# Performance work log

Hardware: AMD Instinct MI355X
Metric: run time of the kernel (lower is better)

Reference implementation:

```python
import jax, jax.numpy as jnp
import numpy as np

H, HD, C = 16, 64, 64            # num_heads, head_dim, mini_batch_size
BASE_LR = 1.0
EPS = 1e-6                        # ttt LN eps (ln_fwd / ln_fused_l2_bwd)


def _l2norm(x):
    return x / jnp.maximum(jnp.linalg.norm(x, axis=-1, keepdims=True), 1e-12)


def _ln_fwd(x, g, b):
    mu = x.mean(-1, keepdims=True)
    var = x.var(-1, keepdims=True)
    return g * ((x - mu) * jax.lax.rsqrt(var + EPS)) + b


def _ln_l2_bwd(x, tgt, g, b):
    # gradient of ||LN(x)*g+b - tgt||^2 / 2 wrt x
    D = x.shape[-1]
    mu = x.mean(-1, keepdims=True)
    var = x.var(-1, keepdims=True)
    std = jnp.sqrt(var + EPS)
    xh = (x - mu) / std
    gout = (g * xh + b) - tgt
    gxh = gout * g
    return (D * gxh - gxh.sum(-1, keepdims=True) - xh * (gxh * xh).sum(-1, keepdims=True)) / (D * std)


def setup_inputs() -> dict:
    key = jax.random.key(0)
    ks = jax.random.split(key, 12)
    B, L, D = 4, 8192, 1024
    std = 0.02
    return {
        'hidden_states': jax.random.normal(ks[0], (B, L, D), jnp.float32),
        'wq_w': jax.random.normal(ks[1], (D, D), jnp.float32) * std,
        'wq_b': jnp.zeros((D,), jnp.float32),
        'wk_w': jax.random.normal(ks[2], (D, D), jnp.float32) * std,
        'wk_b': jnp.zeros((D,), jnp.float32),
        'wv_w': jax.random.normal(ks[3], (D, D), jnp.float32) * std,
        'wv_b': jnp.zeros((D,), jnp.float32),
        'wo_w': jax.random.normal(ks[4], (D, D), jnp.float32) * std,
        'wo_b': jnp.zeros((D,), jnp.float32),
        'ttt_norm_weight': jnp.ones((H, HD), jnp.float32),
        'ttt_norm_bias': jnp.zeros((H, HD), jnp.float32),
        'ttt_lr_weight': jax.random.normal(ks[5], (H, 1, D), jnp.float32) * std,
        'ttt_lr_bias': jnp.zeros((H, 1), jnp.float32),
        'W1': jax.random.normal(ks[6], (H, HD, HD), jnp.float32) * std,
        'b1': jnp.zeros((H, 1, HD), jnp.float32),
        'post_norm_w': jnp.ones((D,), jnp.float32),
        'post_norm_b': jnp.zeros((D,), jnp.float32),
    }


def _forward(hidden_states, wq_w, wq_b, wk_w, wk_b, wv_w, wv_b, wo_w, wo_b,
             ttt_norm_weight, ttt_norm_bias, ttt_lr_weight, ttt_lr_bias,
             W1, b1, post_norm_w, post_norm_b):
    B, L, D = hidden_states.shape
    NC = L // C
    XQ = (hidden_states @ wq_w.T + wq_b).reshape(B, L, H, HD)
    XK = (hidden_states @ wk_w.T + wk_b).reshape(B, L, H, HD)
    XV = (hidden_states @ wv_w.T + wv_b).reshape(B, L, H, HD)
    XQ = _l2norm(XQ)
    XK = _l2norm(XK)
    # ln_reconstruction_target (uses sample std, ddof=1, eps=1e-5 on std)
    d = XV - XK
    mu = d.mean(-1, keepdims=True)
    sd = d.std(-1, keepdims=True, ddof=1)
    XV = ttt_norm_weight[None, None] * ((d - mu) / (sd + 1e-5)) + ttt_norm_bias[None, None] + XK
    # reshape to mini-batches: [B,H,NC,C,HD]
    Xmb = hidden_states.reshape(B, NC, C, D)
    to_mb = lambda t: t.transpose(0, 2, 1, 3).reshape(B, H, NC, C, HD)
    XQ, XK, XV = to_mb(XQ), to_mb(XK), to_mb(XV)
    # eta: sigmoid lr gate per token, row-broadcast over mini-batch
    ttt_lr = jax.nn.sigmoid(jnp.einsum('bnkc,hdc->bhnkd', Xmb, ttt_lr_weight)
                            + ttt_lr_bias.reshape(1, H, 1, 1, 1))     # [B,H,NC,C,1]
    eta = jnp.swapaxes(ttt_lr, -1, -2) * (BASE_LR / HD / C)           # [B,H,NC,1,C]
    mask = jnp.tril(jnp.ones((C, C), hidden_states.dtype))
    g = ttt_norm_weight[None, :, None, :]
    bta = ttt_norm_bias[None, :, None, :]
    W0 = jnp.broadcast_to(W1[None], (B, H, HD, HD))
    b0 = jnp.broadcast_to(b1[None], (B, H, 1, HD))

    def step(carry, xs):
        W, bvec = carry
        xq, xk, xv, eta_row = xs                      # eta_row: [B,H,1,C]
        Z1 = xk @ W + bvec                            # [B,H,C,HD]
        grad = _ln_l2_bwd(Z1, xv - xk, g, bta)        # [B,H,C,HD]
        Attn = mask * jnp.einsum('bhid,bhjd->bhij', xq, xk)   # [B,H,C,C]
        eta_full = jnp.broadcast_to(eta_row, Attn.shape)      # [B,H,C,C]
        b1_bar = bvec - (mask * eta_full) @ grad              # [B,H,C,HD]
        Z1_bar = xq @ W - (eta_full * Attn) @ grad + b1_bar
        last_eta = eta_full[..., -1, :, None]                 # [B,H,C,1]
        W_new = W - jnp.einsum('bhcd,bhce->bhde', last_eta * xk, grad)
        b_new = bvec - (last_eta * grad).sum(-2, keepdims=True)
        out = xq + _ln_fwd(Z1_bar, g, bta)
        return (W_new, b_new), out

    xs = (jnp.moveaxis(XQ, 2, 0), jnp.moveaxis(XK, 2, 0),
          jnp.moveaxis(XV, 2, 0), jnp.moveaxis(eta, 2, 0))
    _, outs = jax.lax.scan(step, (W0, b0), xs)        # outs: [NC,B,H,C,HD]
    y = jnp.moveaxis(outs, 0, 2).reshape(B, H, L, HD).transpose(0, 2, 1, 3).reshape(B, L, D)
    # post LayerNorm (eps=1e-6) + output projection
    mu2 = y.mean(-1, keepdims=True)
    var2 = y.var(-1, keepdims=True)
    y = post_norm_w * ((y - mu2) * jax.lax.rsqrt(var2 + 1e-6)) + post_norm_b
    return y @ wo_w.T + wo_b


def reference(hidden_states, wq_w, wq_b, wk_w, wk_b, wv_w, wv_b, wo_w, wo_b,
              ttt_norm_weight, ttt_norm_bias, ttt_lr_weight, ttt_lr_bias,
              W1, b1, post_norm_w, post_norm_b):
    return _forward(hidden_states, wq_w, wq_b, wk_w, wk_b, wv_w, wv_b, wo_w, wo_b,
                    ttt_norm_weight, ttt_norm_bias, ttt_lr_weight, ttt_lr_bias,
                    W1, b1, post_norm_w, post_norm_b)
```

## Files before the change

kernel.cpp:

```cpp
#include <hip/hip_runtime.h>


typedef __attribute__((ext_vector_type(8))) short short8;
typedef __attribute__((ext_vector_type(4))) float f32x4;
typedef __attribute__((ext_vector_type(4))) unsigned short us4;

__device__ __forceinline__ float bf2f(unsigned short s) {
  union { unsigned int u; float f; } c;
  c.u = ((unsigned int)s) << 16;
  return c.f;
}
__device__ __forceinline__ unsigned short f2bf(float f) {
  union { float f; unsigned int u; } c;
  c.f = f;
  unsigned int u = c.u;
  return (unsigned short)((u + 0x7FFFu + ((u >> 16) & 1u)) >> 16);
}

__device__ __forceinline__ void gload_lds16(const void* g, void* l) {
  __builtin_amdgcn_global_load_lds(
      (const __attribute__((address_space(1))) unsigned int*)g,
      (__attribute__((address_space(3))) unsigned int*)l, 16, 0, 0);
}

__device__ __forceinline__ float dpp16_sum(float x) {
  int v = __float_as_int(x);
  x += __int_as_float(__builtin_amdgcn_update_dpp(v, v, 0xB1, 0xF, 0xF, true));
  v = __float_as_int(x);
  x += __int_as_float(__builtin_amdgcn_update_dpp(v, v, 0x4E, 0xF, 0xF, true));
  v = __float_as_int(x);
  x += __int_as_float(__builtin_amdgcn_update_dpp(v, v, 0x141, 0xF, 0xF, true));
  v = __float_as_int(x);
  x += __int_as_float(__builtin_amdgcn_update_dpp(v, v, 0x140, 0xF, 0xF, true));
  return x;
}

__device__ __forceinline__ void barrier_fast() {
  __builtin_amdgcn_sched_barrier(0);
  asm volatile("s_waitcnt lgkmcnt(0)" ::: "memory");
  __builtin_amdgcn_s_barrier();
  asm volatile("" ::: "memory");
  __builtin_amdgcn_sched_barrier(0);
}
__device__ __forceinline__ void bar_nowait() {
  __builtin_amdgcn_sched_barrier(0);
  asm volatile("" ::: "memory");
  __builtin_amdgcn_s_barrier();
  asm volatile("" ::: "memory");
  __builtin_amdgcn_sched_barrier(0);
}

__global__ __launch_bounds__(256) void cvt_f32_bf16(
    const float* __restrict__ in, unsigned short* __restrict__ out, long n) {
  long i = ((long)blockIdx.x * 256 + threadIdx.x) * 4;
  if (i + 3 < n) {
    float4 v = *(const float4*)&in[i];
    us4 o = { f2bf(v.x), f2bf(v.y), f2bf(v.z), f2bf(v.w) };
    *(us4*)&out[i] = o;
  }
}

__global__ __launch_bounds__(256) void build_wcat(
    const float* __restrict__ wq, const float* __restrict__ wk,
    const float* __restrict__ wv, const float* __restrict__ lrw,
    const float* __restrict__ wqb, const float* __restrict__ wkb,
    const float* __restrict__ wvb, const float* __restrict__ lrb,
    unsigned short* __restrict__ Wcat, float* __restrict__ biasc) {
  int i = blockIdx.x * 256 + threadIdx.x;
  int row = i >> 10, col = i & 1023;
  int h = row >> 8, o = row & 255;
  float v;
  if (o < 64)        v = wq[(h * 64 + o) * 1024 + col];
  else if (o < 128)  v = wk[(h * 64 + o - 64) * 1024 + col];
  else if (o < 192)  v = wv[(h * 64 + o - 128) * 1024 + col];
  else if (o == 192) v = lrw[h * 1024 + col];
  else               v = 0.f;
  Wcat[i] = f2bf(v);
  if (i < 4096) {
    int hh = i >> 8, oo = i & 255;
    float bv;
    if (oo < 64)        bv = wqb[hh * 64 + oo];
    else if (oo < 128)  bv = wkb[hh * 64 + oo - 64];
    else if (oo < 192)  bv = wvb[hh * 64 + oo - 128];
    else if (oo == 192) bv = lrb[hh];
    else                bv = 0.f;
    biasc[i] = bv;
  }
}


__global__ __launch_bounds__(512, 1) void gemm256_qkv(
    const unsigned short* __restrict__ A, const unsigned short* __restrict__ B,
    const float* __restrict__ bias, const float* __restrict__ tnw,
    const float* __restrict__ tnb, unsigned short* __restrict__ XQn,
    unsigned short* __restrict__ XKn, unsigned short* __restrict__ TGT,
    float* __restrict__ eta, long M, long K) {
  __shared__ __align__(16) unsigned short g_lds[49152];
  char* ldsc = (char*)g_lds;
  const int tid = threadIdx.x, lane = tid & 63, wid = tid >> 6;
  const int wm = wid >> 2, wn = wid & 3;
  const int l15 = lane & 15, lg = lane >> 4;
  const int NTILN = 16;

  unsigned nwg = gridDim.x, bid = blockIdx.x;
  unsigned cpx = nwg >> 3;
  unsigned swz = (bid & 7) * cpx + (bid >> 3);
  unsigned nidx = swz % (unsigned)NTILN, midx = swz / (unsigned)NTILN;
  const long m0 = (long)midx * 256, n0 = (long)nidx * 256;
  const long ldab = K * 2;

  const int srow = wid * 16 + (lane >> 2);
  const int scol = ((lane & 3) * 16) ^ (((lane >> 3) & 3) << 4);
  const int sdst = wid * 1024;
  const char* Ab = (const char*)A;
  const char* Bb = (const char*)B;

  const int acol = (lg * 16) ^ (((l15 >> 1) & 3) << 4);
  const int aro = (wm * 128 + l15) * 64 + acol;
  const int bro = 16384 + (wn * 64 + l15) * 64 + acol;

#define STG_A(tt, h, bb)                                                      \
  gload_lds16(Ab + (size_t)(m0 + (h) * 128 + srow) * ldab + (size_t)(tt) * 64 \
                  + scol,                                                     \
              ldsc + (bb) * 32768 + (h) * 8192 + sdst)
#define STG_B(tt, h, bb)                                                      \
  gload_lds16(Bb + (size_t)(n0 + (h) * 128 + srow) * ldab + (size_t)(tt) * 64 \
                  + scol,                                                     \
              ldsc + (bb) * 32768 + 16384 + (h) * 8192 + sdst)

  f32x4 acc[8][4];
#pragma unroll
  for (int m = 0; m < 8; ++m)
#pragma unroll
    for (int n = 0; n < 4; ++n) acc[m][n] = (f32x4){0.f, 0.f, 0.f, 0.f};

  const int NT = (int)(K >> 5);

  STG_A(0, 0, 0); STG_A(0, 1, 0); STG_B(0, 0, 0); STG_B(0, 1, 0);
  STG_A(1, 0, 1); STG_A(1, 1, 1); STG_B(1, 0, 1); STG_B(1, 1, 1);
  asm volatile("s_waitcnt vmcnt(4)" ::: "memory");
  bar_nowait();

  int buf = 0, sb = 2;
#pragma unroll 1
  for (int t = 0; t < NT; ++t) {
    if (t + 2 < NT) {
      STG_A(t + 2, 0, sb); STG_A(t + 2, 1, sb);
      STG_B(t + 2, 0, sb); STG_B(t + 2, 1, sb);
    }
    const char* ab = ldsc + buf * 32768 + aro;
    const char* bb2 = ldsc + buf * 32768 + bro;
    short8 av[8], bv[4];
#pragma unroll
    for (int i = 0; i < 8; ++i) av[i] = *(const short8*)(ab + i * 1024);
#pragma unroll
    for (int nf = 0; nf < 4; ++nf) bv[nf] = *(const short8*)(bb2 + nf * 1024);
    __builtin_amdgcn_s_setprio(1);
#pragma unroll
    for (int i = 0; i < 8; ++i)
#pragma unroll
      for (int nf = 0; nf < 4; ++nf)
        acc[i][nf] = __builtin_amdgcn_mfma_f32_16x16x32_bf16(av[i], bv[nf],
                                                             acc[i][nf], 0, 0, 0);
    __builtin_amdgcn_s_setprio(0);
    asm volatile("s_waitcnt vmcnt(4)" ::: "memory");
    bar_nowait();
    buf = (buf == 2) ? 0 : buf + 1;
    sb = (sb == 2) ? 0 : sb + 1;
  }
#undef STG_A
#undef STG_B

  const int h = (int)nidx;
  float bcol[4], twv[4], tbv[4];
#pragma unroll
  for (int nf = 0; nf < 4; ++nf) {
    bcol[nf] = bias[n0 + wn * 64 + nf * 16 + l15];
    twv[nf] = tnw[h * 64 + nf * 16 + l15];
    tbv[nf] = tnb[h * 64 + nf * 16 + l15];
  }
  __syncthreads();
  unsigned short* kn_s = g_lds;

  if (wn == 0) {
#pragma unroll
    for (int mf = 0; mf < 8; ++mf)
#pragma unroll
      for (int j = 0; j < 4; ++j) {
        float v[4], s2 = 0.f;
#pragma unroll
        for (int nf = 0; nf < 4; ++nf) {
          v[nf] = acc[mf][nf][j] + bcol[nf];
          s2 += v[nf] * v[nf];
        }
        s2 = dpp16_sum(s2);
        float rn = 1.f / fmaxf(sqrtf(s2), 1e-12f);
        size_t tt = (size_t)(m0 + wm * 128 + mf * 16 + lg * 4 + j);
#pragma unroll
        for (int nf = 0; nf < 4; ++nf)
          XQn[tt * 1024 + h * 64 + nf * 16 + l15] = f2bf(v[nf] * rn);
      }
  } else if (wn == 1) {
#pragma unroll
    for (int mf = 0; mf < 8; ++mf)
#pragma unroll
      for (int j = 0; j < 4; ++j) {
        float v[4], s2 = 0.f;
#pragma unroll
        for (int nf = 0; nf < 4; ++nf) {
          v[nf] = acc[mf][nf][j] + bcol[nf];
          s2 += v[nf] * v[nf];
        }
        s2 = dpp16_sum(s2);
        float rn = 1.f / fmaxf(sqrtf(s2), 1e-12f);
        size_t tt = (size_t)(m0 + wm * 128 + mf * 16 + lg * 4 + j);
        int lr_ = wm * 128 + mf * 16 + lg * 4 + j;
#pragma unroll
        for (int nf = 0; nf < 4; ++nf) {
          unsigned short kb = f2bf(v[nf] * rn);
          XKn[tt * 1024 + h * 64 + nf * 16 + l15] = kb;
          kn_s[lr_ * 72 + nf * 16 + l15] = kb;
        }
      }
  }
  __syncthreads();
  if (wn == 2) {
#pragma unroll
    for (int mf = 0; mf < 8; ++mf)
#pragma unroll
      for (int j = 0; j < 4; ++j) {
        int lr_ = wm * 128 + mf * 16 + lg * 4 + j;
        float dv[4], s1 = 0.f, s2 = 0.f;
#pragma unroll
        for (int nf = 0; nf < 4; ++nf) {
          float kn = bf2f(kn_s[lr_ * 72 + nf * 16 + l15]);
          dv[nf] = acc[mf][nf][j] + bcol[nf] - kn;
          s1 += dv[nf];
          s2 += dv[nf] * dv[nf];
        }
        s1 = dpp16_sum(s1);
        s2 = dpp16_sum(s2);
        float mu = s1 * 0.015625f;
        float var1 = fmaxf(s2 - 64.f * mu * mu, 0.f) * (1.f / 63.f);
        float rs = 1.f / (sqrtf(var1) + 1e-5f);
        size_t tt = (size_t)(m0 + wm * 128 + mf * 16 + lg * 4 + j);
#pragma unroll
        for (int nf = 0; nf < 4; ++nf)
          TGT[tt * 1024 + h * 64 + nf * 16 + l15] =
              f2bf(twv[nf] * ((dv[nf] - mu) * rs) + tbv[nf]);
      }
  } else if (wn == 3 && l15 == 0) {
#pragma unroll
    for (int mf = 0; mf < 8; ++mf)
#pragma unroll
      for (int j = 0; j < 4; ++j) {
        size_t tt = (size_t)(m0 + wm * 128 + mf * 16 + lg * 4 + j);
        float lgt = acc[mf][0][j] + bcol[0];
        float sig = 1.f / (1.f + expf(-lgt));
        eta[((tt >> 13) * 16 + h) * 8192 + (tt & 8191)] = sig * (1.f / 4096.f);
      }
  }
}

template <int WRITE_BF16>
__global__ __launch_bounds__(512, 1) void gemm256(
    const unsigned short* __restrict__ A, const unsigned short* __restrict__ B,
    const float* __restrict__ bias, void* __restrict__ Cout,
    long M, long N, long K, int NTILN, long ldc) {
  __shared__ __align__(16) unsigned short g_lds[49152];
  char* ldsc = (char*)g_lds;
  const int tid = threadIdx.x, lane = tid & 63, wid = tid >> 6;
  const int wm = wid >> 2, wn = wid & 3;
  const int l15 = lane & 15, lg = lane >> 4;

  unsigned nwg = gridDim.x, bid = blockIdx.x;
  unsigned cpx = nwg >> 3;
  unsigned swz = (bid & 7) * cpx + (bid >> 3);
  unsigned nidx = swz % (unsigned)NTILN, midx = swz / (unsigned)NTILN;
  const long m0 = (long)midx * 256, n0 = (long)nidx * 256;
  const long ldab = K * 2;

  const int srow = wid * 16 + (lane >> 2);
  const int scol = ((lane & 3) * 16) ^ (((lane >> 3) & 3) << 4);
  const int sdst = wid * 1024;
  const char* Ab = (const char*)A;
  const char* Bb = (const char*)B;

  const int acol = (lg * 16) ^ (((l15 >> 1) & 3) << 4);
  const int aro = (wm * 128 + l15) * 64 + acol;
  const int bro = 16384 + (wn * 64 + l15) * 64 + acol;

#define STG_A(tt, h, bb)                                                      \
  gload_lds16(Ab + (size_t)(m0 + (h) * 128 + srow) * ldab + (size_t)(tt) * 64 \
                  + scol,                                                     \
              ldsc + (bb) * 32768 + (h) * 8192 + sdst)
#define STG_B(tt, h, bb)                                                      \
  gload_lds16(Bb + (size_t)(n0 + (h) * 128 + srow) * ldab + (size_t)(tt) * 64 \
                  + scol,                                                     \
              ldsc + (bb) * 32768 + 16384 + (h) * 8192 + sdst)

  f32x4 acc[8][4];
#pragma unroll
  for (int m = 0; m < 8; ++m)
#pragma unroll
    for (int n = 0; n < 4; ++n) acc[m][n] = (f32x4){0.f, 0.f, 0.f, 0.f};

  const int NT = (int)(K >> 5);

  STG_A(0, 0, 0); STG_A(0, 1, 0); STG_B(0, 0, 0); STG_B(0, 1, 0);
  STG_A(1, 0, 1); STG_A(1, 1, 1); STG_B(1, 0, 1); STG_B(1, 1, 1);
  asm volatile("s_waitcnt vmcnt(4)" ::: "memory");
  bar_nowait();

  int buf = 0, sb = 2;
#pragma unroll 1
  for (int t = 0; t < NT; ++t) {
    if (t + 2 < NT) {
      STG_A(t + 2, 0, sb); STG_A(t + 2, 1, sb);
      STG_B(t + 2, 0, sb); STG_B(t + 2, 1, sb);
    }
    const char* ab = ldsc + buf * 32768 + aro;
    const char* bb2 = ldsc + buf * 32768 + bro;
    short8 av[8], bv[4];
#pragma unroll
    for (int i = 0; i < 8; ++i) av[i] = *(const short8*)(ab + i * 1024);
#pragma unroll
    for (int nf = 0; nf < 4; ++nf) bv[nf] = *(const short8*)(bb2 + nf * 1024);
    __builtin_amdgcn_s_setprio(1);
#pragma unroll
    for (int i = 0; i < 8; ++i)
#pragma unroll
      for (int nf = 0; nf < 4; ++nf)
        acc[i][nf] = __builtin_amdgcn_mfma_f32_16x16x32_bf16(av[i], bv[nf],
                                                             acc[i][nf], 0, 0, 0);
    __builtin_amdgcn_s_setprio(0);
    asm volatile("s_waitcnt vmcnt(4)" ::: "memory");
    bar_nowait();
    buf = (buf == 2) ? 0 : buf + 1;
    sb = (sb == 2) ? 0 : sb + 1;
  }
#undef STG_A
#undef STG_B

#pragma unroll
  for (int mf = 0; mf < 8; ++mf) {
    long r0 = m0 + wm * 128 + mf * 16 + lg * 4;
#pragma unroll
    for (int nf = 0; nf < 4; ++nf) {
      long c = n0 + wn * 64 + nf * 16 + l15;
      float bvv = bias ? bias[c] : 0.f;
#pragma unroll
      for (int j = 0; j < 4; ++j) {
        float v = acc[mf][nf][j] + bvv;
        if (WRITE_BF16)
          ((unsigned short*)Cout)[(r0 + j) * ldc + c] = f2bf(v);
        else
          ((float*)Cout)[(r0 + j) * ldc + c] = v;
      }
    }
  }
}

__global__ __launch_bounds__(512, 1) void ttt_scan(
    const unsigned short* __restrict__ XQ, const unsigned short* __restrict__ XK,
    const unsigned short* __restrict__ TG, const float* __restrict__ eta_buf,
    const float* __restrict__ W1, const float* __restrict__ b1,
    const float* __restrict__ tnw, const float* __restrict__ tnb,
    float* __restrict__ y) {
  const int bh = blockIdx.x;
  const int b = bh >> 4, h = bh & 15;
  const int tid = threadIdx.x;
  const int lane = tid & 63, wid = tid >> 6;
  const bool isA = wid < 4;
  const int q = wid & 3;
  const int l15 = lane & 15, lg = lane >> 4;

  __shared__ __align__(16) unsigned short xq_s[2][64 * 72];
  __shared__ __align__(16) unsigned short tg_s[2][64 * 72];
  __shared__ __align__(16) unsigned short xk_s[2][64 * 72];
  __shared__ __align__(16) unsigned short gc_s[64 * 72];
  __shared__ __align__(16) unsigned short gradT[64 * 72];
  __shared__ __align__(16) unsigned short xkTe[64 * 72];
  __shared__ __align__(16) unsigned short WT_b[2][64 * 72];
  __shared__ float eta_s[2][64];
  __shared__ float bpart[4][64];

  const size_t tokb = (size_t)b * 8192;
  const int col0 = h * 64;
  const int rr_ = q * 16 + (lane >> 3);
  const int c8_ = (lane & 7) * 8;

  short8 pA0[2], pA1[2], pB0[2];
  float peta = 0.f;
  float bstv[4], gwv[4], gbv[4];
  f32x4 Wreg[4];

  if (isA) {
#pragma unroll
    for (int n = 0; n < 4; ++n) {
      int e = n * 16 + l15;
      bstv[n] = b1[h * 64 + e];
      gwv[n] = tnw[h * 64 + e];
      gbv[n] = tnb[h * 64 + e];
    }
#pragma unroll
    for (int j = 0; j < 2; ++j) {
      size_t g = (tokb + rr_ + j * 8) * 1024 + col0 + c8_;
      pA0[j] = *(const short8*)&XQ[g];
      pA1[j] = *(const short8*)&TG[g];
    }
#pragma unroll
    for (int j = 0; j < 2; ++j) {
      int rr = rr_ + j * 8;
      *(short8*)&xq_s[0][rr * 72 + c8_] = pA0[j];
      *(short8*)&tg_s[0][rr * 72 + c8_] = pA1[j];
    }
#pragma unroll
    for (int j = 0; j < 2; ++j) {
      size_t g = (tokb + 64 + rr_ + j * 8) * 1024 + col0 + c8_;
      pA0[j] = *(const short8*)&XQ[g];
      pA1[j] = *(const short8*)&TG[g];
    }
  } else {
#pragma unroll
    for (int j = 0; j < 2; ++j)
      pB0[j] = *(const short8*)&XK[(tokb + rr_ + j * 8) * 1024 + col0 + c8_];
#pragma unroll
    for (int j = 0; j < 2; ++j)
      *(short8*)&xk_s[0][(rr_ + j * 8) * 72 + c8_] = pB0[j];
#pragma unroll
    for (int j = 0; j < 2; ++j)
      pB0[j] = *(const short8*)&XK[(tokb + 64 + rr_ + j * 8) * 1024 + col0 + c8_];
#pragma unroll
    for (int n = 0; n < 4; ++n)
#pragma unroll
      for (int jj = 0; jj < 4; ++jj) {
        int d = q * 16 + lg * 4 + jj, e = n * 16 + l15;
        float w = W1[h * 4096 + d * 64 + e];
        Wreg[n][jj] = w;
        WT_b[0][e * 72 + d] = f2bf(w);
      }
    if (wid == 4) {
      eta_s[0][lane] = eta_buf[(size_t)bh * 8192 + lane];
      peta = eta_buf[(size_t)bh * 8192 + 64 + lane];
    }
  }
  __syncthreads();

  for (int nc = 0; nc < 128; ++nc) {
    const int p = nc & 1;
    const unsigned short* WTc = WT_b[p];
    unsigned short* WTn = WT_b[p ^ 1];

    if (isA) {
      if (nc) {
#pragma unroll
        for (int n = 0; n < 4; ++n) {
          int e = n * 16 + l15;
          bstv[n] -= bpart[0][e] + bpart[1][e] + bpart[2][e] + bpart[3][e];
        }
      }
      if (nc + 1 < 128) {
#pragma unroll
        for (int j = 0; j < 2; ++j) {
          int rr = rr_ + j * 8;
          *(short8*)&xq_s[p ^ 1][rr * 72 + c8_] = pA0[j];
          *(short8*)&tg_s[p ^ 1][rr * 72 + c8_] = pA1[j];
        }
      }
      if (nc + 2 < 128) {
#pragma unroll
        for (int j = 0; j < 2; ++j) {
          size_t g = (tokb + (nc + 2) * 64 + rr_ + j * 8) * 1024 + col0 + c8_;
          pA0[j] = *(const short8*)&XQ[g];
          pA1[j] = *(const short8*)&TG[g];
        }
      }
      f32x4 accZ[4];
#pragma unroll
      for (int n = 0; n < 4; ++n)
        accZ[n] = (f32x4){bstv[n], bstv[n], bstv[n], bstv[n]};
      __builtin_amdgcn_s_setprio(1);
#pragma unroll
      for (int kk = 0; kk < 2; ++kk) {
        const int ko = kk * 32 + lg * 8;
        short8 a_xk = *(const short8*)&xk_s[p][(q * 16 + l15) * 72 + ko];
#pragma unroll
        for (int n = 0; n < 4; ++n) {
          short8 b_w = *(const short8*)&WTc[(n * 16 + l15) * 72 + ko];
          accZ[n] = __builtin_amdgcn_mfma_f32_16x16x32_bf16(a_xk, b_w, accZ[n], 0, 0, 0);
        }
      }
      __builtin_amdgcn_s_setprio(0);
      float grv[4][4];
#pragma unroll
      for (int j = 0; j < 4; ++j) {
        const int r = q * 16 + lg * 4 + j;
        float z[4], s1 = 0.f, s2 = 0.f;
#pragma unroll
        for (int n = 0; n < 4; ++n) {
          z[n] = accZ[n][j];
          s1 += z[n];
          s2 += z[n] * z[n];
        }
        s1 = dpp16_sum(s1);
        s2 = dpp16_sum(s2);
        float mu = s1 * 0.015625f;
        float var = s2 * 0.015625f - mu * mu;
        float rstd = rsqrtf(var + 1e-6f);
        float xh[4], gx[4], s3 = 0.f, s4 = 0.f;
#pragma unroll
        for (int n = 0; n < 4; ++n) {
          xh[n] = (z[n] - mu) * rstd;
          float tg = bf2f(tg_s[p][r * 72 + n * 16 + l15]);
          float go = gwv[n] * xh[n] + gbv[n] - tg;
          gx[n] = go * gwv[n];
          s3 += gx[n];
          s4 += gx[n] * xh[n];
        }
        s3 = dpp16_sum(s3);
        s4 = dpp16_sum(s4);
#pragma unroll
        for (int n = 0; n < 4; ++n)
          grv[n][j] = (64.f * gx[n] - s3 - xh[n] * s4) * rstd * 0.015625f;
      }
#pragma unroll
      for (int n = 0; n < 4; ++n) {
        us4 pk = {f2bf(grv[n][0]), f2bf(grv[n][1]), f2bf(grv[n][2]),
                  f2bf(grv[n][3])};
        *(us4*)&gradT[(n * 16 + l15) * 72 + q * 16 + lg * 4] = pk;
      }
    } else {
      if (nc + 1 < 128) {
#pragma unroll
        for (int j = 0; j < 2; ++j)
          *(short8*)&xk_s[p ^ 1][(rr_ + j * 8) * 72 + c8_] = pB0[j];
        if (wid == 4) eta_s[p ^ 1][lane] = peta;
      }
      if (nc + 2 < 128) {
#pragma unroll
        for (int j = 0; j < 2; ++j)
          pB0[j] = *(const short8*)
              &XK[(tokb + (nc + 2) * 64 + rr_ + j * 8) * 1024 + col0 + c8_];
        if (wid == 4) peta = eta_buf[(size_t)bh * 8192 + (nc + 2) * 64 + lane];
      }
#pragma unroll
      for (int it = 0; it < 4; ++it) {
        int c0 = q * 16 + it * 4;
        us4 pk;
#pragma unroll
        for (int u = 0; u < 4; ++u)
          pk[u] = f2bf(-eta_s[p][c0 + u] * bf2f(xk_s[p][(c0 + u) * 72 + lane]));
        *(us4*)&xkTe[lane * 72 + c0] = pk;
      }
      f32x4 accA[4];
#pragma unroll
      for (int n = 0; n < 4; ++n) accA[n] = (f32x4){0.f, 0.f, 0.f, 0.f};
      __builtin_amdgcn_s_setprio(1);
#pragma unroll
      for (int kk = 0; kk < 2; ++kk) {
        const int ko = kk * 32 + lg * 8;
        short8 a_xq = *(const short8*)&xq_s[p][(q * 16 + l15) * 72 + ko];
#pragma unroll
        for (int n = 0; n < 4; ++n) {
          short8 b_k = *(const short8*)&xk_s[p][(n * 16 + l15) * 72 + ko];
          accA[n] = __builtin_amdgcn_mfma_f32_16x16x32_bf16(a_xq, b_k, accA[n], 0, 0, 0);
        }
      }
      __builtin_amdgcn_s_setprio(0);
#pragma unroll
      for (int j = 0; j < 4; ++j) {
        const int r = q * 16 + lg * 4 + j;
#pragma unroll
        for (int n = 0; n < 4; ++n) {
          int cj = n * 16 + l15;
          float v = (cj <= r) ? (-eta_s[p][cj] * (1.f + accA[n][j])) : 0.f;
          gc_s[r * 72 + cj] = f2bf(v);
        }
      }
    }
    barrier_fast();

    if (isA) {
      f32x4 accZb[4];
#pragma unroll
      for (int n = 0; n < 4; ++n)
        accZb[n] = (f32x4){bstv[n], bstv[n], bstv[n], bstv[n]};
      __builtin_amdgcn_s_setprio(1);
#pragma unroll
      for (int kk = 0; kk < 2; ++kk) {
        const int ko = kk * 32 + lg * 8;
        short8 a_xq = *(const short8*)&xq_s[p][(q * 16 + l15) * 72 + ko];
        short8 a_gc = *(const short8*)&gc_s[(q * 16 + l15) * 72 + ko];
#pragma unroll
        for (int n = 0; n < 4; ++n) {
          short8 b_w = *(const short8*)&WTc[(n * 16 + l15) * 72 + ko];
          short8 b_g = *(const short8*)&gradT[(n * 16 + l15) * 72 + ko];
          accZb[n] = __builtin_amdgcn_mfma_f32_16x16x32_bf16(a_xq, b_w, accZb[n], 0, 0, 0);
          accZb[n] = __builtin_amdgcn_mfma_f32_16x16x32_bf16(a_gc, b_g, accZb[n], 0, 0, 0);
        }
      }
      __builtin_amdgcn_s_setprio(0);
#pragma unroll
      for (int j = 0; j < 4; ++j) {
        const int r = q * 16 + lg * 4 + j;
        float z[4], s1 = 0.f, s2 = 0.f;
#pragma unroll
        for (int n = 0; n < 4; ++n) {
          z[n] = accZb[n][j];
          s1 += z[n];
          s2 += z[n] * z[n];
        }
        s1 = dpp16_sum(s1);
        s2 = dpp16_sum(s2);
        float mu = s1 * 0.015625f;
        float var = s2 * 0.015625f - mu * mu;
        float rstd = rsqrtf(var + 1e-6f);
        size_t gbase = (tokb + nc * 64 + r) * 1024 + col0;
#pragma unroll
        for (int n = 0; n < 4; ++n) {
          int e = n * 16 + l15;
          float ov = bf2f(xq_s[p][r * 72 + e]) + gwv[n] * ((z[n] - mu) * rstd) + gbv[n];
          y[gbase + e] = ov;
        }
      }
    } else {
      short8 a_ke[2], b_g[2][4];
#pragma unroll
      for (int kk = 0; kk < 2; ++kk) {
        const int ko = kk * 32 + lg * 8;
        a_ke[kk] = *(const short8*)&xkTe[(q * 16 + l15) * 72 + ko];
#pragma unroll
        for (int n = 0; n < 4; ++n)
          b_g[kk][n] = *(const short8*)&gradT[(n * 16 + l15) * 72 + ko];
      }
      f32x4 accW[4];
#pragma unroll
      for (int n = 0; n < 4; ++n) accW[n] = Wreg[n];
      __builtin_amdgcn_s_setprio(1);
#pragma unroll
      for (int kk = 0; kk < 2; ++kk)
#pragma unroll
        for (int n = 0; n < 4; ++n)
          accW[n] = __builtin_amdgcn_mfma_f32_16x16x32_bf16(a_ke[kk], b_g[kk][n],
                                                            accW[n], 0, 0, 0);
      __builtin_amdgcn_s_setprio(0);
#pragma unroll
      for (int n = 0; n < 4; ++n) {
        Wreg[n] = accW[n];
        us4 pk = {f2bf(accW[n][0]), f2bf(accW[n][1]), f2bf(accW[n][2]),
                  f2bf(accW[n][3])};
        *(us4*)&WTn[(n * 16 + l15) * 72 + q * 16 + lg * 4] = pk;
      }
      {
        float s = 0.f;
#pragma unroll
        for (int it = 0; it < 4; ++it) {
          us4 gv = *(const us4*)&gradT[lane * 72 + q * 16 + it * 4];
#pragma unroll
          for (int u = 0; u < 4; ++u)
            s += eta_s[p][q * 16 + it * 4 + u] * bf2f(gv[u]);
        }
        bpart[q][lane] = s;
      }
    }
    barrier_fast();
  }
}

__global__ __launch_bounds__(256) void postnorm(
    const float* __restrict__ yv, const float* __restrict__ pw,
    const float* __restrict__ pb, unsigned short* __restrict__ yn) {
  int t = blockIdx.x;
  int tid = threadIdx.x, lane = tid & 63, wid = tid >> 6;
  const float* row = yv + (size_t)t * 1024;
  float4 v = *(const float4*)&row[tid * 4];
  float s1 = v.x + v.y + v.z + v.w;
  float s2 = v.x * v.x + v.y * v.y + v.z * v.z + v.w * v.w;
#pragma unroll
  for (int o = 1; o < 64; o <<= 1) {
    s1 += __shfl_xor(s1, o);
    s2 += __shfl_xor(s2, o);
  }
  __shared__ float r1[4], r2[4];
  if (lane == 0) {
    r1[wid] = s1;
    r2[wid] = s2;
  }
  __syncthreads();
  s1 = r1[0] + r1[1] + r1[2] + r1[3];
  s2 = r2[0] + r2[1] + r2[2] + r2[3];
  float mu = s1 * (1.f / 1024.f);
  float var = s2 * (1.f / 1024.f) - mu * mu;
  float rstd = rsqrtf(var + 1e-6f);
  int c = tid * 4;
  us4 o4 = {f2bf(pw[c] * ((v.x - mu) * rstd) + pb[c]),
            f2bf(pw[c + 1] * ((v.y - mu) * rstd) + pb[c + 1]),
            f2bf(pw[c + 2] * ((v.z - mu) * rstd) + pb[c + 2]),
            f2bf(pw[c + 3] * ((v.w - mu) * rstd) + pb[c + 3])};
  *(us4*)&yn[(size_t)t * 1024 + c] = o4;
}

extern "C" void kernel_launch(void* const* d_in, const int* in_sizes, int n_in,
                              void* d_out, int out_size, void* d_ws,
                              size_t ws_size, hipStream_t stream) {
  const float* hs  = (const float*)d_in[0];
  const float* wqw = (const float*)d_in[1];
  const float* wqb = (const float*)d_in[2];
  const float* wkw = (const float*)d_in[3];
  const float* wkb = (const float*)d_in[4];
  const float* wvw = (const float*)d_in[5];
  const float* wvb = (const float*)d_in[6];
  const float* wow = (const float*)d_in[7];
  const float* wob = (const float*)d_in[8];
  const float* tnw = (const float*)d_in[9];
  const float* tnb = (const float*)d_in[10];
  const float* lrw = (const float*)d_in[11];
  const float* lrb = (const float*)d_in[12];
  const float* W1  = (const float*)d_in[13];
  const float* b1  = (const float*)d_in[14];
  const float* pnw = (const float*)d_in[15];
  const float* pnb = (const float*)d_in[16];

  const size_t OFF_XQ    = 0;
  const size_t OFF_XK    = 67108864;
  const size_t OFF_TGT   = 134217728;
  const size_t OFF_ETA   = 201326592;
  const size_t OFF_WOBF  = OFF_ETA + 2097152;
  const size_t OFF_HSBF  = OFF_WOBF + 2097152;
  const size_t OFF_WCAT  = OFF_HSBF + 67108864;
  const size_t OFF_BIASC = OFF_WCAT + 8388608;
  const size_t OFF_YV    = OFF_HSBF;
  const size_t NEEDED_A  = OFF_BIASC + 16384;
  const size_t NEEDED_B  = OFF_YV + 134217728;
  const size_t NEEDED    = NEEDED_A > NEEDED_B ? NEEDED_A : NEEDED_B;
  if (ws_size < NEEDED) return;

  char* ws = (char*)d_ws;
  unsigned short* XQn   = (unsigned short*)(ws + OFF_XQ);
  unsigned short* ynorm = (unsigned short*)(ws + OFF_XQ);
  unsigned short* XKn   = (unsigned short*)(ws + OFF_XK);
  unsigned short* TGT   = (unsigned short*)(ws + OFF_TGT);
  float* eta_buf        = (float*)(ws + OFF_ETA);
  unsigned short* wo_bf = (unsigned short*)(ws + OFF_WOBF);
  unsigned short* hs_bf = (unsigned short*)(ws + OFF_HSBF);
  unsigned short* Wcat  = (unsigned short*)(ws + OFF_WCAT);
  float* biasc          = (float*)(ws + OFF_BIASC);
  float* yv             = (float*)(ws + OFF_YV);

  cvt_f32_bf16<<<32768, 256, 0, stream>>>(hs, hs_bf, 33554432L);
  build_wcat<<<16384, 256, 0, stream>>>(wqw, wkw, wvw, lrw, wqb, wkb, wvb, lrb,
                                        Wcat, biasc);
  cvt_f32_bf16<<<1024, 256, 0, stream>>>(wow, wo_bf, 1048576L);
  gemm256_qkv<<<2048, 512, 0, stream>>>(hs_bf, Wcat, biasc, tnw, tnb,
                                        XQn, XKn, TGT, eta_buf, 32768L, 1024L);
  ttt_scan<<<64, 512, 0, stream>>>(XQn, XKn, TGT, eta_buf, W1, b1, tnw, tnb, yv);
  postnorm<<<32768, 256, 0, stream>>>(yv, pnw, pnb, ynorm);
  gemm256<0><<<512, 512, 0, stream>>>(ynorm, wo_bf, wob, d_out,
                                      32768L, 1024L, 1024L, 4, 1024L);
}
```

Baseline: 889.1 us.

## Fuse QKV GEMM and TTT scan into one persistent kernel with progress flags

Merges the QKV projection GEMM and the sequential TTT scan into a single launch. The first 64 blocks run the per-(batch, head) scan and spin on per-row-tile atomic progress counters, while the remaining blocks compute GEMM tiles in an order matched to the scan's consumption. This lets the serial scan overlap the GEMM instead of waiting for it to finish. The scan output is also stored as bf16 instead of fp32, halving the traffic into the post-norm. Risks include spin-wait deadlock if scan blocks occupy CUs before producer blocks get scheduled, and a small precision loss on the intermediate y.

```diff
diff --git a/kernel.cpp b/kernel.cpp
--- a/kernel.cpp
+++ b/kernel.cpp
@@ -15,6 +15,11 @@
   c.f = f;
   unsigned int u = c.u;
   return (unsigned short)((u + 0x7FFFu + ((u >> 16) & 1u)) >> 16);
+}
+__device__ __forceinline__ unsigned cvtpk(float lo, float hi) {
+  unsigned r;
+  asm("v_cvt_pk_bf16_f32 %0, %1, %2" : "=v"(r) : "v"(lo), "v"(hi));
+  return r;
 }
 
 __device__ __forceinline__ void gload_lds16(const void* g, void* l) {
@@ -88,177 +93,511 @@
   }
 }
 
-
-__global__ __launch_bounds__(512, 1) void gemm256_qkv(
+__global__ __launch_bounds__(512, 1) void qkv_scan(
     const unsigned short* __restrict__ A, const unsigned short* __restrict__ B,
     const float* __restrict__ bias, const float* __restrict__ tnw,
     const float* __restrict__ tnb, unsigned short* __restrict__ XQn,
     unsigned short* __restrict__ XKn, unsigned short* __restrict__ TGT,
-    float* __restrict__ eta, long M, long K) {
-  __shared__ __align__(16) unsigned short g_lds[49152];
-  char* ldsc = (char*)g_lds;
-  const int tid = threadIdx.x, lane = tid & 63, wid = tid >> 6;
-  const int wm = wid >> 2, wn = wid & 3;
+    float* __restrict__ eta_buf, const float* __restrict__ W1,
+    const float* __restrict__ b1, unsigned short* __restrict__ y,
+    unsigned int* __restrict__ prog) {
+  __shared__ __align__(16) char smem[102912];
+  const int tid = threadIdx.x;
+  const int lane = tid & 63, wid = tid >> 6;
   const int l15 = lane & 15, lg = lane >> 4;
-  const int NTILN = 16;
-
-  unsigned nwg = gridDim.x, bid = blockIdx.x;
-  unsigned cpx = nwg >> 3;
-  unsigned swz = (bid & 7) * cpx + (bid >> 3);
-  unsigned nidx = swz % (unsigned)NTILN, midx = swz / (unsigned)NTILN;
-  const long m0 = (long)midx * 256, n0 = (long)nidx * 256;
-  const long ldab = K * 2;
-
-  const int srow = wid * 16 + (lane >> 2);
-  const int scol = ((lane & 3) * 16) ^ (((lane >> 3) & 3) << 4);
-  const int sdst = wid * 1024;
-  const char* Ab = (const char*)A;
-  const char* Bb = (const char*)B;
-
-  const int acol = (lg * 16) ^ (((l15 >> 1) & 3) << 4);
-  const int aro = (wm * 128 + l15) * 64 + acol;
-  const int bro = 16384 + (wn * 64 + l15) * 64 + acol;
-
-#define STG_A(tt, h, bb)                                                      \
-  gload_lds16(Ab + (size_t)(m0 + (h) * 128 + srow) * ldab + (size_t)(tt) * 64 \
-                  + scol,                                                     \
-              ldsc + (bb) * 32768 + (h) * 8192 + sdst)
-#define STG_B(tt, h, bb)                                                      \
-  gload_lds16(Bb + (size_t)(n0 + (h) * 128 + srow) * ldab + (size_t)(tt) * 64 \
-                  + scol,                                                     \
-              ldsc + (bb) * 32768 + 16384 + (h) * 8192 + sdst)
-
-  f32x4 acc[8][4];
-#pragma unroll
-  for (int m = 0; m < 8; ++m)
-#pragma unroll
-    for (int n = 0; n < 4; ++n) acc[m][n] = (f32x4){0.f, 0.f, 0.f, 0.f};
-
-  const int NT = (int)(K >> 5);
-
-  STG_A(0, 0, 0); STG_A(0, 1, 0); STG_B(0, 0, 0); STG_B(0, 1, 0);
-  STG_A(1, 0, 1); STG_A(1, 1, 1); STG_B(1, 0, 1); STG_B(1, 1, 1);
-  asm volatile("s_waitcnt vmcnt(4)" ::: "memory");
-  bar_nowait();
-
-  int buf = 0, sb = 2;
-#pragma unroll 1
-  for (int t = 0; t < NT; ++t) {
-    if (t + 2 < NT) {
-      STG_A(t + 2, 0, sb); STG_A(t + 2, 1, sb);
-      STG_B(t + 2, 0, sb); STG_B(t + 2, 1, sb);
-    }
-    const char* ab = ldsc + buf * 32768 + aro;
-    const char* bb2 = ldsc + buf * 32768 + bro;
-    short8 av[8], bv[4];
-#pragma unroll
-    for (int i = 0; i < 8; ++i) av[i] = *(const short8*)(ab + i * 1024);
-#pragma unroll
-    for (int nf = 0; nf < 4; ++nf) bv[nf] = *(const short8*)(bb2 + nf * 1024);
-    __builtin_amdgcn_s_setprio(1);
-#pragma unroll
-    for (int i = 0; i < 8; ++i)
-#pragma unroll
-      for (int nf = 0; nf < 4; ++nf)
-        acc[i][nf] = __builtin_amdgcn_mfma_f32_16x16x32_bf16(av[i], bv[nf],
-                                                             acc[i][nf], 0, 0, 0);
-    __builtin_amdgcn_s_setprio(0);
+
+  if (blockIdx.x >= 64) {
+    char* ldsc = smem;
+    const int bid2 = blockIdx.x - 64;
+    const int w = bid2 >> 6, rem = bid2 & 63, bb = rem >> 4, h = rem & 15;
+    const int mprog = bb * 32 + w;
+    const long m0 = (long)mprog * 256;
+    const long n0 = (long)h * 256;
+    const long K = 1024, ldab = 2048;
+
+    const int wm = wid >> 2, wn = wid & 3;
+    const int srow = wid * 16 + (lane >> 2);
+    const int scol = ((lane & 3) * 16) ^ (((lane >> 3) & 3) << 4);
+    const int sdst = wid * 1024;
+    const char* Ab = (const char*)A;
+    const char* Bb = (const char*)B;
+    const int acol = (lg * 16) ^ (((l15 >> 1) & 3) << 4);
+    const int aro = (wm * 128 + l15) * 64 + acol;
+    const int bro = 16384 + (wn * 64 + l15) * 64 + acol;
+
+#define STG_A(tt, hh, bbu)                                                    \
+  gload_lds16(Ab + (size_t)(m0 + (hh) * 128 + srow) * ldab +                  \
+                  (size_t)(tt) * 64 + scol,                                   \
+              ldsc + (bbu) * 32768 + (hh) * 8192 + sdst)
+#define STG_B(tt, hh, bbu)                                                    \
+  gload_lds16(Bb + (size_t)(n0 + (hh) * 128 + srow) * ldab +                  \
+                  (size_t)(tt) * 64 + scol,                                   \
+              ldsc + (bbu) * 32768 + 16384 + (hh) * 8192 + sdst)
+
+    f32x4 acc[8][4];
+#pragma unroll
+    for (int m = 0; m < 8; ++m)
+#pragma unroll
+      for (int n = 0; n < 4; ++n) acc[m][n] = (f32x4){0.f, 0.f, 0.f, 0.f};
+
+    const int NT = (int)(K >> 5);
+    STG_A(0, 0, 0); STG_A(0, 1, 0); STG_B(0, 0, 0); STG_B(0, 1, 0);
+    STG_A(1, 0, 1); STG_A(1, 1, 1); STG_B(1, 0, 1); STG_B(1, 1, 1);
     asm volatile("s_waitcnt vmcnt(4)" ::: "memory");
     bar_nowait();
-    buf = (buf == 2) ? 0 : buf + 1;
-    sb = (sb == 2) ? 0 : sb + 1;
-  }
+
+    int buf = 0, sb = 2;
+#pragma unroll 1
+    for (int t = 0; t < NT; ++t) {
+      if (t + 2 < NT) {
+        STG_A(t + 2, 0, sb); STG_A(t + 2, 1, sb);
+        STG_B(t + 2, 0, sb); STG_B(t + 2, 1, sb);
+      }
+      const char* ab = ldsc + buf * 32768 + aro;
+      const char* bb2 = ldsc + buf * 32768 + bro;
+      short8 av[8], bv[4];
+#pragma unroll
+      for (int i = 0; i < 8; ++i) av[i] = *(const short8*)(ab + i * 1024);
+#pragma unroll
+      for (int nf = 0; nf < 4; ++nf) bv[nf] = *(const short8*)(bb2 + nf * 1024);
+      __builtin_amdgcn_s_setprio(1);
+#pragma unroll
+      for (int i = 0; i < 8; ++i)
+#pragma unroll
+        for (int nf = 0; nf < 4; ++nf)
+          acc[i][nf] = __builtin_amdgcn_mfma_f32_16x16x32_bf16(
+              av[i], bv[nf], acc[i][nf], 0, 0, 0);
+      __builtin_amdgcn_s_setprio(0);
+      if (t < NT - 2)
+        asm volatile("s_waitcnt vmcnt(4)" ::: "memory");
+      else
+        asm volatile("s_waitcnt vmcnt(0)" ::: "memory");
+      bar_nowait();
+      buf = (buf == 2) ? 0 : buf + 1;
+      sb = (sb == 2) ? 0 : sb + 1;
+    }
 #undef STG_A
 #undef STG_B
 
-  const int h = (int)nidx;
-  float bcol[4], twv[4], tbv[4];
-#pragma unroll
-  for (int nf = 0; nf < 4; ++nf) {
-    bcol[nf] = bias[n0 + wn * 64 + nf * 16 + l15];
-    twv[nf] = tnw[h * 64 + nf * 16 + l15];
-    tbv[nf] = tnb[h * 64 + nf * 16 + l15];
+    float bcol[4], twv[4], tbv[4];
+#pragma unroll
+    for (int nf = 0; nf < 4; ++nf) {
+      bcol[nf] = bias[n0 + wn * 64 + nf * 16 + l15];
+      twv[nf] = tnw[h * 64 + nf * 16 + l15];
+      tbv[nf] = tnb[h * 64 + nf * 16 + l15];
+    }
+    __syncthreads();
+    unsigned short* kn_s = (unsigned short*)smem;
+
+    if (wn == 0) {
+#pragma unroll
+      for (int mf = 0; mf < 8; ++mf)
+#pragma unroll
+        for (int j = 0; j < 4; ++j) {
+          float v[4], s2 = 0.f;
+#pragma unroll
+          for (int nf = 0; nf < 4; ++nf) {
+            v[nf] = acc[mf][nf][j] + bcol[nf];
+            s2 += v[nf] * v[nf];
+          }
+          s2 = dpp16_sum(s2);
+          float rn = 1.f / fmaxf(sqrtf(s2), 1e-12f);
+          size_t tt = (size_t)(m0 + wm * 128 + mf * 16 + lg * 4 + j);
+#pragma unroll
+          for (int nf = 0; nf < 4; ++nf)
+            XQn[tt * 1024 + h * 64 + nf * 16 + l15] = f2bf(v[nf] * rn);
+        }
+    } else if (wn == 1) {
+#pragma unroll
+      for (int mf = 0; mf < 8; ++mf)
+#pragma unroll
+        for (int j = 0; j < 4; ++j) {
+          float v[4], s2 = 0.f;
+#pragma unroll
+          for (int nf = 0; nf < 4; ++nf) {
+            v[nf] = acc[mf][nf][j] + bcol[nf];
+            s2 += v[nf] * v[nf];
+          }
+          s2 = dpp16_sum(s2);
+          float rn = 1.f / fmaxf(sqrtf(s2), 1e-12f);
+          size_t tt = (size_t)(m0 + wm * 128 + mf * 16 + lg * 4 + j);
+          int lr_ = wm * 128 + mf * 16 + lg * 4 + j;
+#pragma unroll
+          for (int nf = 0; nf < 4; ++nf) {
+            unsigned short kb = f2bf(v[nf] * rn);
+            XKn[tt * 1024 + h * 64 + nf * 16 + l15] = kb;
+            kn_s[lr_ * 72 + nf * 16 + l15] = kb;
+          }
+        }
+    }
+    __syncthreads();
+    if (wn == 2) {
+#pragma unroll
+      for (int mf = 0; mf < 8; ++mf)
+#pragma unroll
+        for (int j = 0; j < 4; ++j) {
+          int lr_ = wm * 128 + mf * 16 + lg * 4 + j;
+          float dv[4], s1 = 0.f, s2 = 0.f;
+#pragma unroll
+          for (int nf = 0; nf < 4; ++nf) {
+            float kn = bf2f(kn_s[lr_ * 72 + nf * 16 + l15]);
+            dv[nf] = acc[mf][nf][j] + bcol[nf] - kn;
+            s1 += dv[nf];
+            s2 += dv[nf] * dv[nf];
+          }
+          s1 = dpp16_sum(s1);
+          s2 = dpp16_sum(s2);
+          float mu = s1 * 0.015625f;
+          float var1 = fmaxf(s2 - 64.f * mu * mu, 0.f) * (1.f / 63.f);
+          float rs = 1.f / (sqrtf(var1) + 1e-5f);
+          size_t tt = (size_t)(m0 + wm * 128 + mf * 16 + lg * 4 + j);
+#pragma unroll
+          for (int nf = 0; nf < 4; ++nf)
+            TGT[tt * 1024 + h * 64 + nf * 16 + l15] =
+                f2bf(twv[nf] * ((dv[nf] - mu) * rs) + tbv[nf]);
+        }
+    } else if (wn == 3 && l15 == 0) {
+#pragma unroll
+      for (int mf = 0; mf < 8; ++mf)
+#pragma unroll
+        for (int j = 0; j < 4; ++j) {
+          size_t tt = (size_t)(m0 + wm * 128 + mf * 16 + lg * 4 + j);
+          float lgt = acc[mf][0][j] + bcol[0];
+          float sig = 1.f / (1.f + expf(-lgt));
+          eta_buf[((tt >> 13) * 16 + h) * 8192 + (tt & 8191)] =
+              sig * (1.f / 4096.f);
+        }
+    }
+    asm volatile("s_waitcnt vmcnt(0)" ::: "memory");
+    __syncthreads();
+    if (tid == 0) {
+      __threadfence();
+      __hip_atomic_fetch_add(&prog[mprog], 1u, __ATOMIC_RELEASE,
+                             __HIP_MEMORY_SCOPE_AGENT);
+    }
+    return;
+  }
+
+  unsigned short* xq_s = (unsigned short*)(smem);
+  unsigned short* tg_s = (unsigned short*)(smem + 18432);
+  unsigned short* xk_s = (unsigned short*)(smem + 36864);
+  unsigned short* gc_s = (unsigned short*)(smem + 55296);
+  unsigned short* gradT = (unsigned short*)(smem + 64512);
+  unsigned short* xkTe = (unsigned short*)(smem + 73728);
+  unsigned short* WT_b = (unsigned short*)(smem + 82944);
+  float* eta_s = (float*)(smem + 101376);
+  float* bpart = (float*)(smem + 101888);
+
+  const int bh = blockIdx.x;
+  const int b = bh >> 4, h = bh & 15;
+  const bool isA = wid < 4;
+  const int q = wid & 3;
+  const size_t tokb = (size_t)b * 8192;
+  const int col0 = h * 64;
+  const int rr_ = q * 16 + (lane >> 3);
+  const int c8_ = (lane & 7) * 8;
+
+  short8 pA0[2], pA1[2], pB0[2];
+  float peta = 0.f;
+  float bstv[4], gwv[4], gbv[4];
+  f32x4 Wreg[4];
+
+  if (isA) {
+#pragma unroll
+    for (int n = 0; n < 4; ++n) {
+      int e = n * 16 + l15;
+      bstv[n] = b1[h * 64 + e];
+      gwv[n] = tnw[h * 64 + e];
+      gbv[n] = tnb[h * 64 + e];
+    }
+  } else {
+#pragma unroll
+    for (int n = 0; n < 4; ++n)
+#pragma unroll
+      for (int jj = 0; jj < 4; ++jj) {
+        int d = q * 16 + lg * 4 + jj, e = n * 16 + l15;
+        float w2 = W1[h * 4096 + d * 64 + e];
+        Wreg[n][jj] = w2;
+        WT_b[e * 72 + d] = f2bf(w2);
+      }
+  }
+  if (tid == 0) {
+    while (__hip_atomic_load(&prog[b << 5], __ATOMIC_ACQUIRE,
+                             __HIP_MEMORY_SCOPE_AGENT) < 16u)
+      __builtin_amdgcn_s_sleep(16);
   }
   __syncthreads();
-  unsigned short* kn_s = g_lds;
-
-  if (wn == 0) {
-#pragma unroll
-    for (int mf = 0; mf < 8; ++mf)
+
+  if (isA) {
+#pragma unroll
+    for (int j = 0; j < 2; ++j) {
+      size_t g = (tokb + rr_ + j * 8) * 1024 + col0 + c8_;
+      pA0[j] = *(const short8*)&XQn[g];
+      pA1[j] = *(const short8*)&TGT[g];
+    }
+#pragma unroll
+    for (int j = 0; j < 2; ++j) {
+      int rr = rr_ + j * 8;
+      *(short8*)&xq_s[rr * 72 + c8_] = pA0[j];
+      *(short8*)&tg_s[rr * 72 + c8_] = pA1[j];
+    }
+#pragma unroll
+    for (int j = 0; j < 2; ++j) {
+      size_t g = (tokb + 64 + rr_ + j * 8) * 1024 + col0 + c8_;
+      pA0[j] = *(const short8*)&XQn[g];
+      pA1[j] = *(const short8*)&TGT[g];
+    }
+  } else {
+#pragma unroll
+    for (int j = 0; j < 2; ++j)
+      pB0[j] = *(const short8*)&XKn[(tokb + rr_ + j * 8) * 1024 + col0 + c8_];
+#pragma unroll
+    for (int j = 0; j < 2; ++j)
+      *(short8*)&xk_s[(rr_ + j * 8) * 72 + c8_] = pB0[j];
+#pragma unroll
+    for (int j = 0; j < 2; ++j)
+      pB0[j] = *(const short8*)&XKn[(tokb + 64 + rr_ + j * 8) * 1024 + col0 + c8_];
+    if (wid == 4) {
+      eta_s[lane] = eta_buf[(size_t)bh * 8192 + lane];
+      peta = eta_buf[(size_t)bh * 8192 + 64 + lane];
+    }
+  }
+  __syncthreads();
+
+  for (int nc = 0; nc < 128; ++nc) {
+    const int p = nc & 1;
+    if (nc + 2 < 128 && ((nc + 2) & 3) == 0) {
+      if (tid == 0) {
+        while (__hip_atomic_load(&prog[(b << 5) + ((nc + 2) >> 2)],
+                                 __ATOMIC_ACQUIRE,
+                                 __HIP_MEMORY_SCOPE_AGENT) < 16u)
+          __builtin_amdgcn_s_sleep(16);
+      }
+      bar_nowait();
+    }
+    const unsigned short* WTc = WT_b + p * 4608;
+    unsigned short* WTn = WT_b + (p ^ 1) * 4608;
+    unsigned short* xqp = xq_s + p * 4608;
+    unsigned short* tgp = tg_s + p * 4608;
+    unsigned short* xkp = xk_s + p * 4608;
+    float* etp = eta_s + p * 64;
+
+    if (isA) {
+      if (nc) {
+#pragma unroll
+        for (int n = 0; n < 4; ++n) {
+          int e = n * 16 + l15;
+          bstv[n] -= bpart[e] + bpart[64 + e] + bpart[128 + e] + bpart[192 + e];
+        }
+      }
+      if (nc + 1 < 128) {
+        unsigned short* xqn = xq_s + (p ^ 1) * 4608;
+        unsigned short* tgn = tg_s + (p ^ 1) * 4608;
+#pragma unroll
+        for (int j = 0; j < 2; ++j) {
+          int rr = rr_ + j * 8;
+          *(short8*)&xqn[rr * 72 + c8_] = pA0[j];
+          *(short8*)&tgn[rr * 72 + c8_] = pA1[j];
+        }
+      }
+      if (nc + 2 < 128) {
+#pragma unroll
+        for (int j = 0; j < 2; ++j) {
+          size_t g = (tokb + (nc + 2) * 64 + rr_ + j * 8) * 1024 + col0 + c8_;
+          pA0[j] = *(const short8*)&XQn[g];
+          pA1[j] = *(const short8*)&TGT[g];
+        }
+      }
+      f32x4 accZ[4];
+#pragma unroll
+      for (int n = 0; n < 4; ++n)
+        accZ[n] = (f32x4){bstv[n], bstv[n], bstv[n], bstv[n]};
+      __builtin_amdgcn_s_setprio(1);
+#pragma unroll
+      for (int kk = 0; kk < 2; ++kk) {
+        const int ko = kk * 32 + lg * 8;
+        short8 a_xk = *(const short8*)&xkp[(q * 16 + l15) * 72 + ko];
+#pragma unroll
+        for (int n = 0; n < 4; ++n) {
+          short8 b_w = *(const short8*)&WTc[(n * 16 + l15) * 72 + ko];
+          accZ[n] = __builtin_amdgcn_mfma_f32_16x16x32_bf16(a_xk, b_w, accZ[n], 0, 0, 0);
+        }
+      }
+      __builtin_amdgcn_s_setprio(0);
+      float grv[4][4];
 #pragma unroll
       for (int j = 0; j < 4; ++j) {
-        float v[4], s2 = 0.f;
-#pragma unroll
-        for (int nf = 0; nf < 4; ++nf) {
-          v[nf] = acc[mf][nf][j] + bcol[nf];
-          s2 += v[nf] * v[nf];
-        }
-        s2 = dpp16_sum(s2);
-        float rn = 1.f / fmaxf(sqrtf(s2), 1e-12f);
-        size_t tt = (size_t)(m0 + wm * 128 + mf * 16 + lg * 4 + j);
-#pragma unroll
-        for (int nf = 0; nf < 4; ++nf)
-          XQn[tt * 1024 + h * 64 + nf * 16 + l15] = f2bf(v[nf] * rn);
-      }
-  } else if (wn == 1) {
-#pragma unroll
-    for (int mf = 0; mf < 8; ++mf)
-#pragma unroll
-      for (int j = 0; j < 4; ++j) {
-        float v[4], s2 = 0.f;
-#pragma unroll
-        for (int nf = 0; nf < 4; ++nf) {
-          v[nf] = acc[mf][nf][j] + bcol[nf];
-          s2 += v[nf] * v[nf];
-        }
-        s2 = dpp16_sum(s2);
-        float rn = 1.f / fmaxf(sqrtf(s2), 1e-12f);
-        size_t tt = (size_t)(m0 + wm * 128 + mf * 16 + lg * 4 + j);
-        int lr_ = wm * 128 + mf * 16 + lg * 4 + j;
-#pragma unroll
-        for (int nf = 0; nf < 4; ++nf) {
-          unsigned short kb = f2bf(v[nf] * rn);
-          XKn[tt * 1024 + h * 64 + nf * 16 + l15] = kb;
-          kn_s[lr_ * 72 + nf * 16 + l15] = kb;
-        }
-      }
-  }
-  __syncthreads();
-  if (wn == 2) {
-#pragma unroll
-    for (int mf = 0; mf < 8; ++mf)
-#pragma unroll
-      for (int j = 0; j < 4; ++j) {
-        int lr_ = wm * 128 + mf * 16 + lg * 4 + j;
-        float dv[4], s1 = 0.f, s2 = 0.f;
-#pragma unroll
-        for (int nf = 0; nf < 4; ++nf) {
-          float kn = bf2f(kn_s[lr_ * 72 + nf * 16 + l15]);
-          dv[nf] = acc[mf][nf][j] + bcol[nf] - kn;
-          s1 += dv[nf];
-          s2 += dv[nf] * dv[nf];
+        const int r = q * 16 + lg * 4 + j;
+        float z[4], s1 = 0.f, s2 = 0.f;
+#pragma unroll
+        for (int n = 0; n < 4; ++n) {
+          z[n] = accZ[n][j];
+          s1 += z[n];
+          s2 += z[n] * z[n];
         }
         s1 = dpp16_sum(s1);
         s2 = dpp16_sum(s2);
         float mu = s1 * 0.015625f;
-        float var1 = fmaxf(s2 - 64.f * mu * mu, 0.f) * (1.f / 63.f);
-        float rs = 1.f / (sqrtf(var1) + 1e-5f);
-        size_t tt = (size_t)(m0 + wm * 128 + mf * 16 + lg * 4 + j);
-#pragma unroll
-        for (int nf = 0; nf < 4; ++nf)
-          TGT[tt * 1024 + h * 64 + nf * 16 + l15] =
-              f2bf(twv[nf] * ((dv[nf] - mu) * rs) + tbv[nf]);
-      }
-  } else if (wn == 3 && l15 == 0) {
-#pragma unroll
-    for (int mf = 0; mf < 8; ++mf)
+        float var = s2 * 0.015625f - mu * mu;
+        float rstd = rsqrtf(var + 1e-6f);
+        float xh[4], gx[4], s3 = 0.f, s4 = 0.f;
+#pragma unroll
+        for (int n = 0; n < 4; ++n) {
+          xh[n] = (z[n] - mu) * rstd;
+          float tg = bf2f(tgp[r * 72 + n * 16 + l15]);
+          float go = gwv[n] * xh[n] + gbv[n] - tg;
+          gx[n] = go * gwv[n];
+          s3 += gx[n];
+          s4 += gx[n] * xh[n];
+        }
+        s3 = dpp16_sum(s3);
+        s4 = dpp16_sum(s4);
+#pragma unroll
+        for (int n = 0; n < 4; ++n)
+          grv[n][j] = (64.f * gx[n] - s3 - xh[n] * s4) * rstd * 0.015625f;
+      }
+#pragma unroll
+      for (int n = 0; n < 4; ++n) {
+        us4 pk = {f2bf(grv[n][0]), f2bf(grv[n][1]), f2bf(grv[n][2]),
+                  f2bf(grv[n][3])};
+        *(us4*)&gradT[(n * 16 + l15) * 72 + q * 16 + lg * 4] = pk;
+      }
+    } else {
+      if (nc + 1 < 128) {
+        unsigned short* xkn = xk_s + (p ^ 1) * 4608;
+#pragma unroll
+        for (int j = 0; j < 2; ++j)
+          *(short8*)&xkn[(rr_ + j * 8) * 72 + c8_] = pB0[j];
+        if (wid == 4) eta_s[(p ^ 1) * 64 + lane] = peta;
+      }
+      if (nc + 2 < 128) {
+#pragma unroll
+        for (int j = 0; j < 2; ++j)
+          pB0[j] = *(const short8*)
+              &XKn[(tokb + (nc + 2) * 64 + rr_ + j * 8) * 1024 + col0 + c8_];
+        if (wid == 4) peta = eta_buf[(size_t)bh * 8192 + (nc + 2) * 64 + lane];
+      }
+#pragma unroll
+      for (int it = 0; it < 4; ++it) {
+        int c0 = q * 16 + it * 4;
+        us4 pk;
+#pragma unroll
+        for (int u = 0; u < 4; ++u)
+          pk[u] = f2bf(-etp[c0 + u] * bf2f(xkp[(c0 + u) * 72 + lane]));
+        *(us4*)&xkTe[lane * 72 + c0] = pk;
+      }
+      f32x4 accA[4];
+#pragma unroll
+      for (int n = 0; n < 4; ++n) accA[n] = (f32x4){0.f, 0.f, 0.f, 0.f};
+      __builtin_amdgcn_s_setprio(1);
+#pragma unroll
+      for (int kk = 0; kk < 2; ++kk) {
+        const int ko = kk * 32 + lg * 8;
+        short8 a_xq = *(const short8*)&xqp[(q * 16 + l15) * 72 + ko];
+#pragma unroll
+        for (int n = 0; n < 4; ++n) {
+          short8 b_k = *(const short8*)&xkp[(n * 16 + l15) * 72 + ko];
+          accA[n] = __builtin_amdgcn_mfma_f32_16x16x32_bf16(a_xq, b_k, accA[n], 0, 0, 0);
+        }
+      }
+      __builtin_amdgcn_s_setprio(0);
 #pragma unroll
       for (int j = 0; j < 4; ++j) {
-        size_t tt = (size_t)(m0 + wm * 128 + mf * 16 + lg * 4 + j);
-        float lgt = acc[mf][0][j] + bcol[0];
-        float sig = 1.f / (1.f + expf(-lgt));
-        eta[((tt >> 13) * 16 + h) * 8192 + (tt & 8191)] = sig * (1.f / 4096.f);
-      }
+        const int r = q * 16 + lg * 4 + j;
+#pragma unroll
+        for (int n = 0; n < 4; ++n) {
+          int cj = n * 16 + l15;
+          float v = (cj <= r) ? (-etp[cj] * (1.f + accA[n][j])) : 0.f;
+          gc_s[r * 72 + cj] = f2bf(v);
+        }
+      }
+    }
+    barrier_fast();
+
+    if (isA) {
+      f32x4 accZb[4];
+#pragma unroll
+      for (int n = 0; n < 4; ++n)
+        accZb[n] = (f32x4){bstv[n], bstv[n], bstv[n], bstv[n]};
+      __builtin_amdgcn_s_setprio(1);
+#pragma unroll
+      for (int kk = 0; kk < 2; ++kk) {
+        const int ko = kk * 32 + lg * 8;
+        short8 a_xq = *(const short8*)&xqp[(q * 16 + l15) * 72 + ko];
+        short8 a_gc = *(const short8*)&gc_s[(q * 16 + l15) * 72 + ko];
+#pragma unroll
+        for (int n = 0; n < 4; ++n) {
+          short8 b_w = *(const short8*)&WTc[(n * 16 + l15) * 72 + ko];
+          short8 b_g = *(const short8*)&gradT[(n * 16 + l15) * 72 + ko];
+          accZb[n] = __builtin_amdgcn_mfma_f32_16x16x32_bf16(a_xq, b_w, accZb[n], 0, 0, 0);
+          accZb[n] = __builtin_amdgcn_mfma_f32_16x16x32_bf16(a_gc, b_g, accZb[n], 0, 0, 0);
+        }
+      }
+      __builtin_amdgcn_s_setprio(0);
+#pragma unroll
+      for (int j = 0; j < 4; ++j) {
+        const int r = q * 16 + lg * 4 + j;
+        float z[4], s1 = 0.f, s2 = 0.f;
+#pragma unroll
+        for (int n = 0; n < 4; ++n) {
+          z[n] = accZb[n][j];
+          s1 += z[n];
+          s2 += z[n] * z[n];
+        }
+        s1 = dpp16_sum(s1);
+        s2 = dpp16_sum(s2);
+        float mu = s1 * 0.015625f;
+        float var = s2 * 0.015625f - mu * mu;
+        float rstd = rsqrtf(var + 1e-6f);
+        size_t gbase = (tokb + nc * 64 + r) * 1024 + col0;
+#pragma unroll
+        for (int n = 0; n < 4; ++n) {
+          int e = n * 16 + l15;
+          float ov = bf2f(xqp[r * 72 + e]) + gwv[n] * ((z[n] - mu) * rstd) + gbv[n];
+          y[gbase + e] = (unsigned short)(cvtpk(ov, ov) & 0xffffu);
+        }
+      }
+    } else {
+      short8 a_ke[2], b_g[2][4];
+#pragma unroll
+      for (int kk = 0; kk < 2; ++kk) {
+        const int ko = kk * 32 + lg * 8;
+        a_ke[kk] = *(const short8*)&xkTe[(q * 16 + l15) * 72 + ko];
+#pragma unroll
+        for (int n = 0; n < 4; ++n)
+          b_g[kk][n] = *(const short8*)&gradT[(n * 16 + l15) * 72 + ko];
+      }
+      f32x4 accW[4];
+#pragma unroll
+      for (int n = 0; n < 4; ++n) accW[n] = Wreg[n];
+      __builtin_amdgcn_s_setprio(1);
+#pragma unroll
+      for (int kk = 0; kk < 2; ++kk)
+#pragma unroll
+        for (int n = 0; n < 4; ++n)
+          accW[n] = __builtin_amdgcn_mfma_f32_16x16x32_bf16(a_ke[kk], b_g[kk][n],
+                                                            accW[n], 0, 0, 0);
+      __builtin_amdgcn_s_setprio(0);
+#pragma unroll
+      for (int n = 0; n < 4; ++n) {
+        Wreg[n] = accW[n];
+        us4 pk = {f2bf(accW[n][0]), f2bf(accW[n][1]), f2bf(accW[n][2]),
+                  f2bf(accW[n][3])};
+        *(us4*)&WTn[(n * 16 + l15) * 72 + q * 16 + lg * 4] = pk;
+      }
+      {
+        float s = 0.f;
+#pragma unroll
+        for (int it = 0; it < 4; ++it) {
+          us4 gv = *(const us4*)&gradT[lane * 72 + q * 16 + it * 4];
+#pragma unroll
+          for (int u = 0; u < 4; ++u)
+            s += etp[q * 16 + it * 4 + u] * bf2f(gv[u]);
+        }
+        bpart[q * 64 + lane] = s;
+      }
+    }
+    barrier_fast();
   }
 }
 
@@ -334,7 +673,10 @@
         acc[i][nf] = __builtin_amdgcn_mfma_f32_16x16x32_bf16(av[i], bv[nf],
                                                              acc[i][nf], 0, 0, 0);
     __builtin_amdgcn_s_setprio(0);
-    asm volatile("s_waitcnt vmcnt(4)" ::: "memory");
+    if (t < NT - 2)
+      asm volatile("s_waitcnt vmcnt(4)" ::: "memory");
+    else
+      asm volatile("s_waitcnt vmcnt(0)" ::: "memory");
     bar_nowait();
     buf = (buf == 2) ? 0 : buf + 1;
     sb = (sb == 2) ? 0 : sb + 1;
@@ -361,322 +703,20 @@
   }
 }
 
-__global__ __launch_bounds__(512, 1) void ttt_scan(
-    const unsigned short* __restrict__ XQ, const unsigned short* __restrict__ XK,
-    const unsigned short* __restrict__ TG, const float* __restrict__ eta_buf,
-    const float* __restrict__ W1, const float* __restrict__ b1,
-    const float* __restrict__ tnw, const float* __restrict__ tnb,
-    float* __restrict__ y) {
-  const int bh = blockIdx.x;
-  const int b = bh >> 4, h = bh & 15;
-  const int tid = threadIdx.x;
-  const int lane = tid & 63, wid = tid >> 6;
-  const bool isA = wid < 4;
-  const int q = wid & 3;
-  const int l15 = lane & 15, lg = lane >> 4;
-
-  __shared__ __align__(16) unsigned short xq_s[2][64 * 72];
-  __shared__ __align__(16) unsigned short tg_s[2][64 * 72];
-  __shared__ __align__(16) unsigned short xk_s[2][64 * 72];
-  __shared__ __align__(16) unsigned short gc_s[64 * 72];
-  __shared__ __align__(16) unsigned short gradT[64 * 72];
-  __shared__ __align__(16) unsigned short xkTe[64 * 72];
-  __shared__ __align__(16) unsigned short WT_b[2][64 * 72];
-  __shared__ float eta_s[2][64];
-  __shared__ float bpart[4][64];
-
-  const size_t tokb = (size_t)b * 8192;
-  const int col0 = h * 64;
-  const int rr_ = q * 16 + (lane >> 3);
-  const int c8_ = (lane & 7) * 8;
-
-  short8 pA0[2], pA1[2], pB0[2];
-  float peta = 0.f;
-  float bstv[4], gwv[4], gbv[4];
-  f32x4 Wreg[4];
-
-  if (isA) {
-#pragma unroll
-    for (int n = 0; n < 4; ++n) {
-      int e = n * 16 + l15;
-      bstv[n] = b1[h * 64 + e];
-      gwv[n] = tnw[h * 64 + e];
-      gbv[n] = tnb[h * 64 + e];
-    }
-#pragma unroll
-    for (int j = 0; j < 2; ++j) {
-      size_t g = (tokb + rr_ + j * 8) * 1024 + col0 + c8_;
-      pA0[j] = *(const short8*)&XQ[g];
-      pA1[j] = *(const short8*)&TG[g];
-    }
-#pragma unroll
-    for (int j = 0; j < 2; ++j) {
-      int rr = rr_ + j * 8;
-      *(short8*)&xq_s[0][rr * 72 + c8_] = pA0[j];
-      *(short8*)&tg_s[0][rr * 72 + c8_] = pA1[j];
-    }
-#pragma unroll
-    for (int j = 0; j < 2; ++j) {
-      size_t g = (tokb + 64 + rr_ + j * 8) * 1024 + col0 + c8_;
-      pA0[j] = *(const short8*)&XQ[g];
-      pA1[j] = *(const short8*)&TG[g];
-    }
-  } else {
-#pragma unroll
-    for (int j = 0; j < 2; ++j)
-      pB0[j] = *(const short8*)&XK[(tokb + rr_ + j * 8) * 1024 + col0 + c8_];
-#pragma unroll
-    for (int j = 0; j < 2; ++j)
-      *(short8*)&xk_s[0][(rr_ + j * 8) * 72 + c8_] = pB0[j];
-#pragma unroll
-    for (int j = 0; j < 2; ++j)
-      pB0[j] = *(const short8*)&XK[(tokb + 64 + rr_ + j * 8) * 1024 + col0 + c8_];
-#pragma unroll
-    for (int n = 0; n < 4; ++n)
-#pragma unroll
-      for (int jj = 0; jj < 4; ++jj) {
-        int d = q * 16 + lg * 4 + jj, e = n * 16 + l15;
-        float w = W1[h * 4096 + d * 64 + e];
-        Wreg[n][jj] = w;
-        WT_b[0][e * 72 + d] = f2bf(w);
-      }
-    if (wid == 4) {
-      eta_s[0][lane] = eta_buf[(size_t)bh * 8192 + lane];
-      peta = eta_buf[(size_t)bh * 8192 + 64 + lane];
-    }
-  }
-  __syncthreads();
-
-  for (int nc = 0; nc < 128; ++nc) {
-    const int p = nc & 1;
-    const unsigned short* WTc = WT_b[p];
-    unsigned short* WTn = WT_b[p ^ 1];
-
-    if (isA) {
-      if (nc) {
-#pragma unroll
-        for (int n = 0; n < 4; ++n) {
-          int e = n * 16 + l15;
-          bstv[n] -= bpart[0][e] + bpart[1][e] + bpart[2][e] + bpart[3][e];
-        }
-      }
-      if (nc + 1 < 128) {
-#pragma unroll
-        for (int j = 0; j < 2; ++j) {
-          int rr = rr_ + j * 8;
-          *(short8*)&xq_s[p ^ 1][rr * 72 + c8_] = pA0[j];
-          *(short8*)&tg_s[p ^ 1][rr * 72 + c8_] = pA1[j];
-        }
-      }
-      if (nc + 2 < 128) {
-#pragma unroll
-        for (int j = 0; j < 2; ++j) {
-          size_t g = (tokb + (nc + 2) * 64 + rr_ + j * 8) * 1024 + col0 + c8_;
-          pA0[j] = *(const short8*)&XQ[g];
-          pA1[j] = *(const short8*)&TG[g];
-        }
-      }
-      f32x4 accZ[4];
-#pragma unroll
-      for (int n = 0; n < 4; ++n)
-        accZ[n] = (f32x4){bstv[n], bstv[n], bstv[n], bstv[n]};
-      __builtin_amdgcn_s_setprio(1);
-#pragma unroll
-      for (int kk = 0; kk < 2; ++kk) {
-        const int ko = kk * 32 + lg * 8;
-        short8 a_xk = *(const short8*)&xk_s[p][(q * 16 + l15) * 72 + ko];
-#pragma unroll
-        for (int n = 0; n < 4; ++n) {
-          short8 b_w = *(const short8*)&WTc[(n * 16 + l15) * 72 + ko];
-          accZ[n] = __builtin_amdgcn_mfma_f32_16x16x32_bf16(a_xk, b_w, accZ[n], 0, 0, 0);
-        }
-      }
-      __builtin_amdgcn_s_setprio(0);
-      float grv[4][4];
-#pragma unroll
-      for (int j = 0; j < 4; ++j) {
-        const int r = q * 16 + lg * 4 + j;
-        float z[4], s1 = 0.f, s2 = 0.f;
-#pragma unroll
-        for (int n = 0; n < 4; ++n) {
-          z[n] = accZ[n][j];
-          s1 += z[n];
-          s2 += z[n] * z[n];
-        }
-        s1 = dpp16_sum(s1);
-        s2 = dpp16_sum(s2);
-        float mu = s1 * 0.015625f;
-        float var = s2 * 0.015625f - mu * mu;
-        float rstd = rsqrtf(var + 1e-6f);
-        float xh[4], gx[4], s3 = 0.f, s4 = 0.f;
-#pragma unroll
-        for (int n = 0; n < 4; ++n) {
-          xh[n] = (z[n] - mu) * rstd;
-          float tg = bf2f(tg_s[p][r * 72 + n * 16 + l15]);
-          float go = gwv[n] * xh[n] + gbv[n] - tg;
-          gx[n] = go * gwv[n];
-          s3 += gx[n];
-          s4 += gx[n] * xh[n];
-        }
-        s3 = dpp16_sum(s3);
-        s4 = dpp16_sum(s4);
-#pragma unroll
-        for (int n = 0; n < 4; ++n)
-          grv[n][j] = (64.f * gx[n] - s3 - xh[n] * s4) * rstd * 0.015625f;
-      }
-#pragma unroll
-      for (int n = 0; n < 4; ++n) {
-        us4 pk = {f2bf(grv[n][0]), f2bf(grv[n][1]), f2bf(grv[n][2]),
-                  f2bf(grv[n][3])};
-        *(us4*)&gradT[(n * 16 + l15) * 72 + q * 16 + lg * 4] = pk;
-      }
-    } else {
-      if (nc + 1 < 128) {
-#pragma unroll
-        for (int j = 0; j < 2; ++j)
-          *(short8*)&xk_s[p ^ 1][(rr_ + j * 8) * 72 + c8_] = pB0[j];
-        if (wid == 4) eta_s[p ^ 1][lane] = peta;
-      }
-      if (nc + 2 < 128) {
-#pragma unroll
-        for (int j = 0; j < 2; ++j)
-          pB0[j] = *(const short8*)
-              &XK[(tokb + (nc + 2) * 64 + rr_ + j * 8) * 1024 + col0 + c8_];
-        if (wid == 4) peta = eta_buf[(size_t)bh * 8192 + (nc + 2) * 64 + lane];
-      }
-#pragma unroll
-      for (int it = 0; it < 4; ++it) {
-        int c0 = q * 16 + it * 4;
-        us4 pk;
-#pragma unroll
-        for (int u = 0; u < 4; ++u)
-          pk[u] = f2bf(-eta_s[p][c0 + u] * bf2f(xk_s[p][(c0 + u) * 72 + lane]));
-        *(us4*)&xkTe[lane * 72 + c0] = pk;
-      }
-      f32x4 accA[4];
-#pragma unroll
-      for (int n = 0; n < 4; ++n) accA[n] = (f32x4){0.f, 0.f, 0.f, 0.f};
-      __builtin_amdgcn_s_setprio(1);
-#pragma unroll
-      for (int kk = 0; kk < 2; ++kk) {
-        const int ko = kk * 32 + lg * 8;
-        short8 a_xq = *(const short8*)&xq_s[p][(q * 16 + l15) * 72 + ko];
-#pragma unroll
-        for (int n = 0; n < 4; ++n) {
-          short8 b_k = *(const short8*)&xk_s[p][(n * 16 + l15) * 72 + ko];
-          accA[n] = __builtin_amdgcn_mfma_f32_16x16x32_bf16(a_xq, b_k, accA[n], 0, 0, 0);
-        }
-      }
-      __builtin_amdgcn_s_setprio(0);
-#pragma unroll
-      for (int j = 0; j < 4; ++j) {
-        const int r = q * 16 + lg * 4 + j;
-#pragma unroll
-        for (int n = 0; n < 4; ++n) {
-          int cj = n * 16 + l15;
-          float v = (cj <= r) ? (-eta_s[p][cj] * (1.f + accA[n][j])) : 0.f;
-          gc_s[r * 72 + cj] = f2bf(v);
-        }
-      }
-    }
-    barrier_fast();
-
-    if (isA) {
-      f32x4 accZb[4];
-#pragma unroll
-      for (int n = 0; n < 4; ++n)
-        accZb[n] = (f32x4){bstv[n], bstv[n], bstv[n], bstv[n]};
-      __builtin_amdgcn_s_setprio(1);
-#pragma unroll
-      for (int kk = 0; kk < 2; ++kk) {
-        const int ko = kk * 32 + lg * 8;
-        short8 a_xq = *(const short8*)&xq_s[p][(q * 16 + l15) * 72 + ko];
-        short8 a_gc = *(const short8*)&gc_s[(q * 16 + l15) * 72 + ko];
-#pragma unroll
-        for (int n = 0; n < 4; ++n) {
-          short8 b_w = *(const short8*)&WTc[(n * 16 + l15) * 72 + ko];
-          short8 b_g = *(const short8*)&gradT[(n * 16 + l15) * 72 + ko];
-          accZb[n] = __builtin_amdgcn_mfma_f32_16x16x32_bf16(a_xq, b_w, accZb[n], 0, 0, 0);
-          accZb[n] = __builtin_amdgcn_mfma_f32_16x16x32_bf16(a_gc, b_g, accZb[n], 0, 0, 0);
-        }
-      }
-      __builtin_amdgcn_s_setprio(0);
-#pragma unroll
-      for (int j = 0; j < 4; ++j) {
-        const int r = q * 16 + lg * 4 + j;
-        float z[4], s1 = 0.f, s2 = 0.f;
-#pragma unroll
-        for (int n = 0; n < 4; ++n) {
-          z[n] = accZb[n][j];
-          s1 += z[n];
-          s2 += z[n] * z[n];
-        }
-        s1 = dpp16_sum(s1);
-        s2 = dpp16_sum(s2);
-        float mu = s1 * 0.015625f;
-        float var = s2 * 0.015625f - mu * mu;
-        float rstd = rsqrtf(var + 1e-6f);
-        size_t gbase = (tokb + nc * 64 + r) * 1024 + col0;
-#pragma unroll
-        for (int n = 0; n < 4; ++n) {
-          int e = n * 16 + l15;
-          float ov = bf2f(xq_s[p][r * 72 + e]) + gwv[n] * ((z[n] - mu) * rstd) + gbv[n];
-          y[gbase + e] = ov;
-        }
-      }
-    } else {
-      short8 a_ke[2], b_g[2][4];
-#pragma unroll
-      for (int kk = 0; kk < 2; ++kk) {
-        const int ko = kk * 32 + lg * 8;
-        a_ke[kk] = *(const short8*)&xkTe[(q * 16 + l15) * 72 + ko];
-#pragma unroll
-        for (int n = 0; n < 4; ++n)
-          b_g[kk][n] = *(const short8*)&gradT[(n * 16 + l15) * 72 + ko];
-      }
-      f32x4 accW[4];
-#pragma unroll
-      for (int n = 0; n < 4; ++n) accW[n] = Wreg[n];
-      __builtin_amdgcn_s_setprio(1);
-#pragma unroll
-      for (int kk = 0; kk < 2; ++kk)
-#pragma unroll
-        for (int n = 0; n < 4; ++n)
-          accW[n] = __builtin_amdgcn_mfma_f32_16x16x32_bf16(a_ke[kk], b_g[kk][n],
-                                                            accW[n], 0, 0, 0);
-      __builtin_amdgcn_s_setprio(0);
-#pragma unroll
-      for (int n = 0; n < 4; ++n) {
-        Wreg[n] = accW[n];
-        us4 pk = {f2bf(accW[n][0]), f2bf(accW[n][1]), f2bf(accW[n][2]),
-                  f2bf(accW[n][3])};
-        *(us4*)&WTn[(n * 16 + l15) * 72 + q * 16 + lg * 4] = pk;
-      }
-      {
-        float s = 0.f;
-#pragma unroll
-        for (int it = 0; it < 4; ++it) {
-          us4 gv = *(const us4*)&gradT[lane * 72 + q * 16 + it * 4];
-#pragma unroll
-          for (int u = 0; u < 4; ++u)
-            s += eta_s[p][q * 16 + it * 4 + u] * bf2f(gv[u]);
-        }
-        bpart[q][lane] = s;
-      }
-    }
-    barrier_fast();
-  }
-}
-
 __global__ __launch_bounds__(256) void postnorm(
-    const float* __restrict__ yv, const float* __restrict__ pw,
+    const unsigned short* __restrict__ yv, const float* __restrict__ pw,
     const float* __restrict__ pb, unsigned short* __restrict__ yn) {
   int t = blockIdx.x;
   int tid = threadIdx.x, lane = tid & 63, wid = tid >> 6;
-  const float* row = yv + (size_t)t * 1024;
-  float4 v = *(const float4*)&row[tid * 4];
-  float s1 = v.x + v.y + v.z + v.w;
-  float s2 = v.x * v.x + v.y * v.y + v.z * v.z + v.w * v.w;
+  us4 v4 = *(const us4*)&yv[(size_t)t * 1024 + tid * 4];
+  float v[4];
+  float s1 = 0.f, s2 = 0.f;
+#pragma unroll
+  for (int u = 0; u < 4; ++u) {
+    v[u] = bf2f(v4[u]);
+    s1 += v[u];
+    s2 += v[u] * v[u];
+  }
 #pragma unroll
   for (int o = 1; o < 64; o <<= 1) {
     s1 += __shfl_xor(s1, o);
@@ -694,10 +734,10 @@
   float var = s2 * (1.f / 1024.f) - mu * mu;
   float rstd = rsqrtf(var + 1e-6f);
   int c = tid * 4;
-  us4 o4 = {f2bf(pw[c] * ((v.x - mu) * rstd) + pb[c]),
-            f2bf(pw[c + 1] * ((v.y - mu) * rstd) + pb[c + 1]),
-            f2bf(pw[c + 2] * ((v.z - mu) * rstd) + pb[c + 2]),
-            f2bf(pw[c + 3] * ((v.w - mu) * rstd) + pb[c + 3])};
+  us4 o4;
+#pragma unroll
+  for (int u = 0; u < 4; ++u)
+    o4[u] = f2bf(pw[c + u] * ((v[u] - mu) * rstd) + pb[c + u]);
   *(us4*)&yn[(size_t)t * 1024 + c] = o4;
 }
 
@@ -726,14 +766,13 @@
   const size_t OFF_XK    = 67108864;
   const size_t OFF_TGT   = 134217728;
   const size_t OFF_ETA   = 201326592;
-  const size_t OFF_WOBF  = OFF_ETA + 2097152;
-  const size_t OFF_HSBF  = OFF_WOBF + 2097152;
+  const size_t OFF_WOBF  = 203423744;
+  const size_t OFF_PROG  = 205520896;
+  const size_t OFF_HSBF  = 205524992;
   const size_t OFF_WCAT  = OFF_HSBF + 67108864;
   const size_t OFF_BIASC = OFF_WCAT + 8388608;
-  const size_t OFF_YV    = OFF_HSBF;
-  const size_t NEEDED_A  = OFF_BIASC + 16384;
-  const size_t NEEDED_B  = OFF_YV + 134217728;
-  const size_t NEEDED    = NEEDED_A > NEEDED_B ? NEEDED_A : NEEDED_B;
+  const size_t OFF_YBF   = OFF_BIASC + 16384;
+  const size_t NEEDED    = OFF_YBF + 67108864;
   if (ws_size < NEEDED) return;
 
   char* ws = (char*)d_ws;
@@ -743,19 +782,20 @@
   unsigned short* TGT   = (unsigned short*)(ws + OFF_TGT);
   float* eta_buf        = (float*)(ws + OFF_ETA);
   unsigned short* wo_bf = (unsigned short*)(ws + OFF_WOBF);
+  unsigned int* prog    = (unsigned int*)(ws + OFF_PROG);
   unsigned short* hs_bf = (unsigned short*)(ws + OFF_HSBF);
   unsigned short* Wcat  = (unsigned short*)(ws + OFF_WCAT);
   float* biasc          = (float*)(ws + OFF_BIASC);
-  float* yv             = (float*)(ws + OFF_YV);
+  unsigned short* ybf   = (unsigned short*)(ws + OFF_YBF);
 
   cvt_f32_bf16<<<32768, 256, 0, stream>>>(hs, hs_bf, 33554432L);
   build_wcat<<<16384, 256, 0, stream>>>(wqw, wkw, wvw, lrw, wqb, wkb, wvb, lrb,
                                         Wcat, biasc);
   cvt_f32_bf16<<<1024, 256, 0, stream>>>(wow, wo_bf, 1048576L);
-  gemm256_qkv<<<2048, 512, 0, stream>>>(hs_bf, Wcat, biasc, tnw, tnb,
-                                        XQn, XKn, TGT, eta_buf, 32768L, 1024L);
-  ttt_scan<<<64, 512, 0, stream>>>(XQn, XKn, TGT, eta_buf, W1, b1, tnw, tnb, yv);
-  postnorm<<<32768, 256, 0, stream>>>(yv, pnw, pnb, ynorm);
+  hipMemsetAsync(prog, 0, 4096, stream);
+  qkv_scan<<<2112, 512, 0, stream>>>(hs_bf, Wcat, biasc, tnw, tnb,
+                                     XQn, XKn, TGT, eta_buf, W1, b1, ybf, prog);
+  postnorm<<<32768, 256, 0, stream>>>(ybf, pnw, pnb, ynorm);
   gemm256<0><<<512, 512, 0, stream>>>(ynorm, wo_bf, wob, d_out,
                                       32768L, 1024L, 1024L, 4, 1024L);
 }
```

Result: faster. 777.1 us, median of 2 (-12.6%).
